# Performance work log

Hardware: AMD Instinct MI355X
Metric: run time of the kernel (lower is better)

The kernel has to match this reference:

```python
import jax, jax.numpy as jnp
import numpy as np

S, B, T, E, H, VS, VT = 40, 32, 40, 256, 512, 50000, 50000
PAD = 0


def lstm_cell(x, h, c, Wih, Whh, b):
    # PyTorch gate order: i, f, g, o
    g = x @ Wih.T + h @ Whh.T + b
    i, f, gg, o = jnp.split(g, 4, axis=-1)
    c = jax.nn.sigmoid(f) * c + jax.nn.sigmoid(i) * jnp.tanh(gg)
    h = jax.nn.sigmoid(o) * jnp.tanh(c)
    return h, c


def run_lstm(xs, Wih, Whh, b):
    # xs: [S, B, E] -> hs [S, B, H], final (h, c)
    b_ = xs.shape[1]
    init = (jnp.zeros((b_, H), xs.dtype), jnp.zeros((b_, H), xs.dtype))
    def step(carry, x):
        h, c = lstm_cell(x, carry[0], carry[1], Wih, Whh, b)
        return (h, c), h
    (hT, cT), hs = jax.lax.scan(step, init, xs)
    return hs, hT, cT


def setup_inputs() -> dict:
    key = jax.random.key(0)
    ks = jax.random.split(key, 20)
    w = lambda k, shp: (jax.random.normal(k, shp, dtype=jnp.float32) * 0.05)
    return {
        "padded_source": jax.random.randint(ks[0], (S, B), 0, VS, dtype=jnp.int32),
        "padded_target": jax.random.randint(ks[1], (T, B), 0, VT, dtype=jnp.int32),
        "enc_masks": jnp.zeros((B, S), dtype=jnp.float32),
        "src_embed": w(ks[2], (VS, E)),
        "tgt_embed": w(ks[3], (VT, E)),
        "enc_Wih_f": w(ks[4], (4 * H, E)),
        "enc_Whh_f": w(ks[5], (4 * H, H)),
        "enc_b_f": w(ks[6], (4 * H,)),
        "enc_Wih_b": w(ks[7], (4 * H, E)),
        "enc_Whh_b": w(ks[8], (4 * H, H)),
        "enc_b_b": w(ks[9], (4 * H,)),
        "dec_Wih": w(ks[10], (4 * H, E + H)),
        "dec_Whh": w(ks[11], (4 * H, H)),
        "dec_b": w(ks[12], (4 * H,)),
        "W_h": w(ks[13], (H, 2 * H)),
        "W_c": w(ks[14], (H, 2 * H)),
        "W_att": w(ks[15], (H, 2 * H)),
        "W_comb": w(ks[16], (H, 3 * H)),
        "W_vocab": w(ks[17], (VT, H)),
    }


def reference(padded_source, padded_target, enc_masks, src_embed, tgt_embed,
              enc_Wih_f, enc_Whh_f, enc_b_f, enc_Wih_b, enc_Whh_b, enc_b_b,
              dec_Wih, dec_Whh, dec_b, W_h, W_c, W_att, W_comb, W_vocab):
    # ---- encode ----
    src_e = src_embed[padded_source]                      # [S, B, E]
    hs_f, hT_f, cT_f = run_lstm(src_e, enc_Wih_f, enc_Whh_f, enc_b_f)
    hs_b, hT_b, cT_b = run_lstm(src_e[::-1], enc_Wih_b, enc_Whh_b, enc_b_b)
    hs_b = hs_b[::-1]
    enc_hidden = jnp.concatenate([hs_f, hs_b], axis=-1).transpose(1, 0, 2)  # [B, S, 2H]
    dec_h = jnp.concatenate([hT_f, hT_b], axis=-1) @ W_h.T  # [B, H]
    dec_c = jnp.concatenate([cT_f, cT_b], axis=-1) @ W_c.T
    enc_proj = enc_hidden @ W_att.T                        # [B, S, H]

    # ---- decode (scan over target timesteps) ----
    tgt_e = tgt_embed[padded_target[:-1]]                  # [T-1, B, E]
    o0 = jnp.zeros((enc_hidden.shape[0], H), enc_hidden.dtype)

    def dstep(carry, emb_t):
        h, c, o_prev = carry
        x = jnp.concatenate([emb_t, o_prev], axis=-1)
        h, c = lstm_cell(x, h, c, dec_Wih, dec_Whh, dec_b)
        scores = jnp.einsum('bsh,bh->bs', enc_proj, h)
        scores = jnp.where(enc_masks > 0, -jnp.inf, scores)
        att = jax.nn.softmax(scores, axis=-1)
        ctx = jnp.einsum('bs,bsd->bd', att, enc_hidden)
        o_t = jnp.tanh(jnp.concatenate([h, ctx], axis=-1) @ W_comb.T)
        return (h, c, o_t), o_t

    _, outs = jax.lax.scan(dstep, (dec_h, dec_c, o0), tgt_e)  # [T-1, B, H]

    # ---- scoring ----
    logp = jax.nn.log_softmax(outs @ W_vocab.T, axis=-1)      # [T-1, B, VT]
    tgt = padded_target[1:]
    tmask = (tgt != PAD).astype(logp.dtype)
    picked = jnp.take_along_axis(logp, tgt[..., None], axis=-1)[..., 0] * tmask
    return picked.sum(axis=0)                                  # [B]
```

## Files before the change

kernel.cpp:

```cpp
#include <hip/hip_runtime.h>
#include <hip/hip_cooperative_groups.h>
#include <math.h>

namespace cg = cooperative_groups;


#define S_LEN 40
#define BATCH 32
#define EMB   256
#define HID   512
#define G4H   2048
#define NVOC  50000
#define NDEC  39
#define NCHUNK 196
#define MROWS 1248
#define MPAD  1280

__device__ __forceinline__ float sigf(float x) { return 1.f / (1.f + expf(-x)); }

__global__ __launch_bounds__(256) void k_embed(
    const int* __restrict__ src_ids, const int* __restrict__ tgt_ids,
    const float* __restrict__ src_emb, const float* __restrict__ tgt_emb,
    float* __restrict__ src_e, float* __restrict__ tgt_e)
{
  int row = blockIdx.x, tid = threadIdx.x;
  if (row < S_LEN*BATCH) {
    int id = src_ids[row];
    src_e[(size_t)row*EMB + tid] = src_emb[(size_t)id*EMB + tid];
  } else {
    int r = row - S_LEN*BATCH;
    int id = tgt_ids[r];
    tgt_e[(size_t)r*EMB + tid] = tgt_emb[(size_t)id*EMB + tid];
  }
}

__global__ __launch_bounds__(256) void k_gemm(
    const float* __restrict__ A, const float* __restrict__ W,
    const float* __restrict__ bias, float* __restrict__ C,
    int N, int K, int ldw, int rev)
{
  __shared__ float As[16][36];
  __shared__ float Ws[16][256];
  const int tid = threadIdx.x;
  const int tx = tid & 31, ty = tid >> 5;
  const int bn = (int)blockIdx.x << 8;
  const int bmi = (int)blockIdx.y;
  const int bm = bmi << 5;
  const int arow0 = rev ? ((S_LEN - 1 - bmi) << 5) : bm;

  float acc[4][8];
#pragma unroll
  for (int i = 0; i < 4; i++)
#pragma unroll
    for (int j = 0; j < 8; j++) acc[i][j] = 0.f;

  const int ml = tid >> 3, kl = (tid & 7) << 1;
  const float* aptr = A + (size_t)(arow0 + ml)*K + kl;
  const float* wptr = W + (size_t)(bn + tid)*ldw;

  for (int k0 = 0; k0 < K; k0 += 16) {
    const float2 av  = *(const float2*)(aptr + k0);
    const float4 w0v = *(const float4*)(wptr + k0);
    const float4 w1v = *(const float4*)(wptr + k0 + 4);
    const float4 w2v = *(const float4*)(wptr + k0 + 8);
    const float4 w3v = *(const float4*)(wptr + k0 + 12);
    __syncthreads();
    As[kl][ml]   = av.x;
    As[kl+1][ml] = av.y;
    const float wt[16] = {w0v.x,w0v.y,w0v.z,w0v.w, w1v.x,w1v.y,w1v.z,w1v.w,
                          w2v.x,w2v.y,w2v.z,w2v.w, w3v.x,w3v.y,w3v.z,w3v.w};
#pragma unroll
    for (int kk = 0; kk < 16; kk++) Ws[kk][tid] = wt[kk];
    __syncthreads();
#pragma unroll
    for (int kk = 0; kk < 16; kk++) {
      const float4 a4 = *(const float4*)&As[kk][ty << 2];
      const float4 b0 = *(const float4*)&Ws[kk][tx << 2];
      const float4 b1 = *(const float4*)&Ws[kk][128 + (tx << 2)];
      const float ar[4] = {a4.x, a4.y, a4.z, a4.w};
      const float br[8] = {b0.x, b0.y, b0.z, b0.w, b1.x, b1.y, b1.z, b1.w};
#pragma unroll
      for (int i = 0; i < 4; i++)
#pragma unroll
        for (int j = 0; j < 8; j++) acc[i][j] += ar[i]*br[j];
    }
  }
  float4 bb0 = {0,0,0,0}, bb1 = {0,0,0,0};
  if (bias) {
    bb0 = *(const float4*)&bias[bn + (tx << 2)];
    bb1 = *(const float4*)&bias[bn + 128 + (tx << 2)];
  }
#pragma unroll
  for (int i = 0; i < 4; i++) {
    const int row = bm + (ty << 2) + i;
    float4 o0 = {acc[i][0]+bb0.x, acc[i][1]+bb0.y, acc[i][2]+bb0.z, acc[i][3]+bb0.w};
    float4 o1 = {acc[i][4]+bb1.x, acc[i][5]+bb1.y, acc[i][6]+bb1.z, acc[i][7]+bb1.w};
    *(float4*)&C[(size_t)row*N + bn + (tx << 2)] = o0;
    *(float4*)&C[(size_t)row*N + bn + 128 + (tx << 2)] = o1;
  }
}

__global__ __launch_bounds__(256) void k_enc(
    const float* __restrict__ xpf, const float* __restrict__ xpb,
    const float* __restrict__ Whf, const float* __restrict__ Whb,
    float* __restrict__ hpf, float* __restrict__ hpb,
    float* __restrict__ hcat, float* __restrict__ ccat)
{
  cg::grid_group grid = cg::this_grid();
  const int blk = blockIdx.x;
  const int dir = blk >> 7;
  const int ub  = blk & 127;
  const int tid = threadIdx.x;
  const int w = tid >> 6, lane = tid & 63;
  const int r = lane & 31, half = lane >> 5;
  const int j = ub*4 + w;
  const int kbase = half << 8;

  const float* xp  = dir ? xpb : xpf;
  const float* Whh = dir ? Whb : Whf;
  float* hp = dir ? hpb : hpf;

  const float* w0 = Whh + (size_t)(0*HID + j)*HID + kbase;
  const float* w1 = Whh + (size_t)(1*HID + j)*HID + kbase;
  const float* w2 = Whh + (size_t)(2*HID + j)*HID + kbase;
  const float* w3 = Whh + (size_t)(3*HID + j)*HID + kbase;

  float creg = 0.f;
  for (int t = 0; t < S_LEN; t++) {
    float a0 = 0.f, a1 = 0.f, a2 = 0.f, a3 = 0.f;
    if (t > 0) {
      const float* hb = hp + (size_t)(t-1)*16384 + (kbase << 5) + (r << 2);
#pragma unroll 4
      for (int kk = 0; kk < 256; kk += 4) {
        const float4 hv = *(const float4*)(hb + (kk << 5));
        const float4 v0 = *(const float4*)(w0 + kk);
        const float4 v1 = *(const float4*)(w1 + kk);
        const float4 v2 = *(const float4*)(w2 + kk);
        const float4 v3 = *(const float4*)(w3 + kk);
        a0 += v0.x*hv.x + v0.y*hv.y + v0.z*hv.z + v0.w*hv.w;
        a1 += v1.x*hv.x + v1.y*hv.y + v1.z*hv.z + v1.w*hv.w;
        a2 += v2.x*hv.x + v2.y*hv.y + v2.z*hv.z + v2.w*hv.w;
        a3 += v3.x*hv.x + v3.y*hv.y + v3.z*hv.z + v3.w*hv.w;
      }
    }
    a0 += __shfl_down(a0, 32);
    a1 += __shfl_down(a1, 32);
    a2 += __shfl_down(a2, 32);
    a3 += __shfl_down(a3, 32);
    if (half == 0) {
      const float* xrow = xp + (size_t)(t*BATCH + r)*G4H;
      const float gi = a0 + xrow[j];
      const float gf = a1 + xrow[HID + j];
      const float gg = a2 + xrow[2*HID + j];
      const float go = a3 + xrow[3*HID + j];
      const float cn = sigf(gf)*creg + sigf(gi)*tanhf(gg);
      const float hn = sigf(go)*tanhf(cn);
      creg = cn;
      hp[(size_t)t*16384 + (j >> 2)*128 + (r << 2) + (j & 3)] = hn;
      if (t == S_LEN-1) {
        hcat[r*1024 + dir*HID + j] = hn;
        ccat[r*1024 + dir*HID + j] = cn;
      }
    }
    grid.sync();
  }
}

__global__ __launch_bounds__(256) void k_concat(
    const float* __restrict__ hpf, const float* __restrict__ hpb,
    float* __restrict__ ench)
{
  const int blk = blockIdx.x, tid = threadIdx.x;
  const int b = blk / S_LEN, s = blk - b*S_LEN;
#pragma unroll
  for (int q = 0; q < 4; q++) {
    const int d = tid + (q << 8);
    float v;
    if (d < HID) v = hpf[(size_t)s*16384 + (d >> 2)*128 + (b << 2) + (d & 3)];
    else {
      const int d2 = d - HID;
      v = hpb[(size_t)(S_LEN-1-s)*16384 + (d2 >> 2)*128 + (b << 2) + (d2 & 3)];
    }
    ench[(size_t)blk*1024 + d] = v;
  }
}

__global__ __launch_bounds__(256) void k_dec(
    const float* __restrict__ xproj, const float* __restrict__ Wih, const float* __restrict__ Whh,
    const float* __restrict__ Wcomb, const float* __restrict__ encp, const float* __restrict__ ench,
    const float* __restrict__ masks, const float* __restrict__ h0, const float* __restrict__ c0,
    float* __restrict__ aop, float* __restrict__ xcomb, float* __restrict__ outs)
{
  cg::grid_group grid = cg::this_grid();
  __shared__ float redA[4][2][4][32];
  __shared__ float redC[4][2][32];
  __shared__ float hl[HID];
  __shared__ float sc[S_LEN];

  const int blk = blockIdx.x, tid = threadIdx.x;
  const int w = tid >> 6, lane = tid & 63;
  const int r = lane & 31, half = lane >> 5;
  const int j0 = blk*2;

  const int kbA = w*256 + half*128;
  const float* wA[8];
#pragma unroll
  for (int u = 0; u < 2; u++)
#pragma unroll
    for (int g = 0; g < 4; g++) {
      const int row = g*HID + j0 + u;
      wA[u*4+g] = (kbA < HID) ? (Wih + (size_t)row*768 + 256 + kbA)
                              : (Whh + (size_t)row*HID + (kbA - HID));
    }
  const float* habase = aop + (kbA << 5) + (r << 2);

  const int kbC = w*384 + half*192;
  const float* wC0 = Wcomb + (size_t)(j0  )*1536 + kbC;
  const float* wC1 = Wcomb + (size_t)(j0+1)*1536 + kbC;
  const float* hcbase = xcomb + (kbC << 5) + (r << 2);

  float creg = 0.f;
  if (tid < 64) {
    const int uh = tid >> 5, rr = tid & 31;
    const int j = j0 + uh;
    creg = c0[rr*HID + j];
    aop[(128 + (j >> 2))*128 + (rr << 2) + (j & 3)] = h0[rr*HID + j];
    aop[((j >> 2))*128 + (rr << 2) + (j & 3)] = 0.f;
  }
  grid.sync();

  for (int t = 0; t < NDEC; t++) {
    {
      float acc8[8];
#pragma unroll
      for (int p = 0; p < 8; p++) acc8[p] = 0.f;
#pragma unroll 2
      for (int kk = 0; kk < 128; kk += 4) {
        const float4 hv = *(const float4*)(habase + (kk << 5));
#pragma unroll
        for (int p = 0; p < 8; p++) {
          const float4 wv = *(const float4*)(wA[p] + kk);
          acc8[p] += wv.x*hv.x + wv.y*hv.y + wv.z*hv.z + wv.w*hv.w;
        }
      }
#pragma unroll
      for (int p = 0; p < 8; p++) acc8[p] += __shfl_down(acc8[p], 32);
      if (half == 0) {
#pragma unroll
        for (int p = 0; p < 8; p++) redA[w][p >> 2][p & 3][r] = acc8[p];
      }
    }
    __syncthreads();
    if (tid < 64) {
      const int uh = tid >> 5, rr = tid & 31, j = j0 + uh;
      const float* xrow = xproj + (size_t)(t*BATCH + rr)*G4H;
      float g4[4];
#pragma unroll
      for (int g = 0; g < 4; g++)
        g4[g] = xrow[g*HID + j] + redA[0][uh][g][rr] + redA[1][uh][g][rr]
                                + redA[2][uh][g][rr] + redA[3][uh][g][rr];
      const float cn = sigf(g4[1])*creg + sigf(g4[0])*tanhf(g4[2]);
      const float hn = sigf(g4[3])*tanhf(cn);
      creg = cn;
      xcomb[(j >> 2)*128 + (rr << 2) + (j & 3)] = hn;
      aop[(128 + (j >> 2))*128 + (rr << 2) + (j & 3)] = hn;
    }
    grid.sync();

    if (blk < BATCH) {
      const int b = blk;
      if (tid < 128) ((float4*)hl)[tid] = *(const float4*)&xcomb[tid*128 + (b << 2)];
      __syncthreads();
      for (int s = w; s < S_LEN; s += 4) {
        const float* ep = encp + ((size_t)b*S_LEN + s)*HID;
        float part = 0.f;
#pragma unroll
        for (int k = 0; k < 8; k++) part += ep[lane + (k << 6)]*hl[lane + (k << 6)];
#pragma unroll
        for (int m = 32; m >= 1; m >>= 1) part += __shfl_xor(part, m, 64);
        if (lane == 0) sc[s] = (masks[b*S_LEN + s] > 0.f) ? -INFINITY : part;
      }
      __syncthreads();
      float mx = -INFINITY;
      for (int s2 = 0; s2 < S_LEN; s2++) mx = fmaxf(mx, sc[s2]);
      float sm = 0.f;
      for (int s2 = 0; s2 < S_LEN; s2++) sm += expf(sc[s2] - mx);
      const float inv = 1.f/sm;
      const float myatt = (tid < S_LEN) ? expf(sc[tid] - mx)*inv : 0.f;
      __syncthreads();
      if (tid < S_LEN) sc[tid] = myatt;
      __syncthreads();
#pragma unroll
      for (int q = 0; q < 4; q++) {
        const int d = tid + (q << 8);
        float cd = 0.f;
        for (int s = 0; s < S_LEN; s++) cd += sc[s]*ench[((size_t)b*S_LEN + s)*1024 + d];
        const int k = HID + d;
        xcomb[(k >> 2)*128 + (b << 2) + (k & 3)] = cd;
      }
    }
    grid.sync();

    {
      float ca = 0.f, cb = 0.f;
#pragma unroll 2
      for (int kk = 0; kk < 192; kk += 4) {
        const float4 hv = *(const float4*)(hcbase + (kk << 5));
        const float4 v0 = *(const float4*)(wC0 + kk);
        const float4 v1 = *(const float4*)(wC1 + kk);
        ca += v0.x*hv.x + v0.y*hv.y + v0.z*hv.z + v0.w*hv.w;
        cb += v1.x*hv.x + v1.y*hv.y + v1.z*hv.z + v1.w*hv.w;
      }
      ca += __shfl_down(ca, 32);
      cb += __shfl_down(cb, 32);
      if (half == 0) { redC[w][0][r] = ca; redC[w][1][r] = cb; }
    }
    __syncthreads();
    if (tid < 64) {
      const int uh = tid >> 5, rr = tid & 31, j = j0 + uh;
      const float o = tanhf(redC[0][uh][rr] + redC[1][uh][rr] + redC[2][uh][rr] + redC[3][uh][rr]);
      aop[(j >> 2)*128 + (rr << 2) + (j & 3)] = o;
      outs[(size_t)(t*BATCH + rr)*HID + j] = o;
    }
    grid.sync();
  }
}

__global__ __launch_bounds__(256) void k_vocab(
    const float* __restrict__ A, const float* __restrict__ W,
    const int* __restrict__ ptgt,
    float* __restrict__ pmax, float* __restrict__ psum, float* __restrict__ picked)
{
  __shared__ float As[16][68];
  __shared__ float Ws[16][256];
  const int tid = threadIdx.x;
  const int tx = tid & 31, ty = tid >> 5;
  const int bn = (int)blockIdx.x << 8;
  const int bm = (int)blockIdx.y << 6;

  float acc[8][8];
#pragma unroll
  for (int i = 0; i < 8; i++)
#pragma unroll
    for (int j = 0; j < 8; j++) acc[i][j] = 0.f;

  const int ml = tid >> 2, kl = (tid & 3) << 2;
  const float* aptr = A + (size_t)(bm + ml)*HID + kl;
  int wrow = bn + tid; if (wrow >= NVOC) wrow = NVOC - 1;
  const float* wptr = W + (size_t)wrow*HID;

  for (int k0 = 0; k0 < HID; k0 += 16) {
    const float4 av  = *(const float4*)(aptr + k0);
    const float4 w0v = *(const float4*)(wptr + k0);
    const float4 w1v = *(const float4*)(wptr + k0 + 4);
    const float4 w2v = *(const float4*)(wptr + k0 + 8);
    const float4 w3v = *(const float4*)(wptr + k0 + 12);
    __syncthreads();
    As[kl][ml] = av.x; As[kl+1][ml] = av.y; As[kl+2][ml] = av.z; As[kl+3][ml] = av.w;
    const float wt[16] = {w0v.x,w0v.y,w0v.z,w0v.w, w1v.x,w1v.y,w1v.z,w1v.w,
                          w2v.x,w2v.y,w2v.z,w2v.w, w3v.x,w3v.y,w3v.z,w3v.w};
#pragma unroll
    for (int kk = 0; kk < 16; kk++) Ws[kk][tid] = wt[kk];
    __syncthreads();
#pragma unroll
    for (int kk = 0; kk < 16; kk++) {
      const float4 a0 = *(const float4*)&As[kk][ty << 3];
      const float4 a1 = *(const float4*)&As[kk][(ty << 3) + 4];
      const float4 b0 = *(const float4*)&Ws[kk][tx << 2];
      const float4 b1 = *(const float4*)&Ws[kk][128 + (tx << 2)];
      const float ar[8] = {a0.x,a0.y,a0.z,a0.w, a1.x,a1.y,a1.z,a1.w};
      const float br[8] = {b0.x,b0.y,b0.z,b0.w, b1.x,b1.y,b1.z,b1.w};
#pragma unroll
      for (int i = 0; i < 8; i++)
#pragma unroll
        for (int j = 0; j < 8; j++) acc[i][j] += ar[i]*br[j];
    }
  }
#pragma unroll
  for (int i = 0; i < 8; i++) {
    const int row = bm + (ty << 3) + i;
    float mx = -INFINITY;
#pragma unroll
    for (int j = 0; j < 8; j++) {
      const int col = bn + ((j < 4) ? (tx << 2) + j : 128 + (tx << 2) + j - 4);
      if (col < NVOC) mx = fmaxf(mx, acc[i][j]);
    }
#pragma unroll
    for (int m = 16; m >= 1; m >>= 1) mx = fmaxf(mx, __shfl_xor(mx, m, 32));
    float sm = 0.f;
#pragma unroll
    for (int j = 0; j < 8; j++) {
      const int col = bn + ((j < 4) ? (tx << 2) + j : 128 + (tx << 2) + j - 4);
      if (col < NVOC) sm += expf(acc[i][j] - mx);
    }
#pragma unroll
    for (int m = 16; m >= 1; m >>= 1) sm += __shfl_xor(sm, m, 32);
    if (tx == 0) {
      pmax[(size_t)row*NCHUNK + blockIdx.x] = mx;
      psum[(size_t)row*NCHUNK + blockIdx.x] = sm;
    }
    if (row < MROWS) {
      const int tt = row >> 5, bb = row & 31;
      const int tv = ptgt[(tt + 1)*BATCH + bb];
      const int rel = tv - bn;
      if (rel >= 0 && rel < 256) {
#pragma unroll
        for (int j = 0; j < 8; j++) {
          const int cl = (j < 4) ? (tx << 2) + j : 128 + (tx << 2) + j - 4;
          if (cl == rel) picked[row] = acc[i][j];
        }
      }
    }
  }
}

__global__ __launch_bounds__(256) void k_final(
    const float* __restrict__ pmax, const float* __restrict__ psum,
    const float* __restrict__ picked, const int* __restrict__ ptgt,
    float* __restrict__ out)
{
  __shared__ float red[8];
  const int b = (int)blockIdx.x, tid = threadIdx.x;
  const int lane = tid & 63, w = tid >> 6;
  float accum = 0.f;
  for (int t = 0; t < NDEC; t++) {
    const int row = t*BATCH + b;
    const float* pm = pmax + (size_t)row*NCHUNK;
    const float* ps = psum + (size_t)row*NCHUNK;
    float mx = -INFINITY;
    for (int c = tid; c < NCHUNK; c += 256) mx = fmaxf(mx, pm[c]);
#pragma unroll
    for (int m = 32; m >= 1; m >>= 1) mx = fmaxf(mx, __shfl_xor(mx, m, 64));
    if (lane == 0) red[w] = mx;
    __syncthreads();
    mx = fmaxf(fmaxf(red[0], red[1]), fmaxf(red[2], red[3]));
    __syncthreads();
    float sm = 0.f;
    for (int c = tid; c < NCHUNK; c += 256) sm += ps[c]*expf(pm[c] - mx);
#pragma unroll
    for (int m = 32; m >= 1; m >>= 1) sm += __shfl_xor(sm, m, 64);
    if (lane == 0) red[w] = sm;
    __syncthreads();
    sm = red[0] + red[1] + red[2] + red[3];
    __syncthreads();
    if (tid == 0) {
      const int tv = ptgt[(t + 1)*BATCH + b];
      if (tv != 0) accum += picked[row] - (mx + logf(sm));
    }
  }
  if (tid == 0) out[b] = accum;
}

extern "C" void kernel_launch(void* const* d_in, const int* in_sizes, int n_in,
                              void* d_out, int out_size, void* d_ws, size_t ws_size,
                              hipStream_t stream) {
  (void)in_sizes; (void)n_in; (void)out_size; (void)ws_size;
  const int*   p_src     = (const int*)d_in[0];
  const int*   p_tgt     = (const int*)d_in[1];
  const float* enc_masks = (const float*)d_in[2];
  const float* src_embed = (const float*)d_in[3];
  const float* tgt_embed = (const float*)d_in[4];
  const float* Wih_f = (const float*)d_in[5];
  const float* Whh_f = (const float*)d_in[6];
  const float* b_f   = (const float*)d_in[7];
  const float* Wih_b = (const float*)d_in[8];
  const float* Whh_b = (const float*)d_in[9];
  const float* b_b   = (const float*)d_in[10];
  const float* dWih  = (const float*)d_in[11];
  const float* dWhh  = (const float*)d_in[12];
  const float* db    = (const float*)d_in[13];
  const float* W_h   = (const float*)d_in[14];
  const float* W_c   = (const float*)d_in[15];
  const float* W_att = (const float*)d_in[16];
  const float* W_comb= (const float*)d_in[17];
  const float* W_voc = (const float*)d_in[18];
  float* out = (float*)d_out;

  float* p = (float*)d_ws;
  float* src_e    = p; p += S_LEN*BATCH*EMB;
  float* tgt_e    = p; p += NDEC*BATCH*EMB;
  float* xpf      = p; p += S_LEN*BATCH*G4H;
  float* xpb      = p; p += S_LEN*BATCH*G4H;
  float* dec_xp   = p; p += NDEC*BATCH*G4H;
  float* hpf      = p; p += S_LEN*BATCH*HID;
  float* hpb      = p; p += S_LEN*BATCH*HID;
  float* hcat     = p; p += BATCH*2*HID;
  float* ccat     = p; p += BATCH*2*HID;
  float* ench     = p; p += BATCH*S_LEN*2*HID;
  float* encp     = p; p += BATCH*S_LEN*HID;
  float* h0       = p; p += BATCH*HID;
  float* c0       = p; p += BATCH*HID;
  float* aop      = p; p += 1024*BATCH;
  float* xcomb    = p; p += 1536*BATCH;
  float* outs     = p; p += (size_t)MPAD*HID;
  float* pmaxb    = p; p += (size_t)MPAD*NCHUNK;
  float* psumb    = p; p += (size_t)MPAD*NCHUNK;
  float* pickedb  = p; p += MPAD;

  k_embed<<<S_LEN*BATCH + NDEC*BATCH, 256, 0, stream>>>(p_src, p_tgt, src_embed, tgt_embed, src_e, tgt_e);

  k_gemm<<<dim3(8, 40), 256, 0, stream>>>(src_e, Wih_f, b_f, xpf, G4H, EMB, EMB, 0);
  k_gemm<<<dim3(8, 40), 256, 0, stream>>>(src_e, Wih_b, b_b, xpb, G4H, EMB, EMB, 1);
  k_gemm<<<dim3(8, NDEC), 256, 0, stream>>>(tgt_e, dWih, db, dec_xp, G4H, EMB, 768, 0);

  {
    void* args[] = { (void*)&xpf, (void*)&xpb, (void*)&Whh_f, (void*)&Whh_b,
                     (void*)&hpf, (void*)&hpb, (void*)&hcat, (void*)&ccat };
    hipLaunchCooperativeKernel((void*)k_enc, dim3(256), dim3(256), args, 0, stream);
  }

  k_concat<<<BATCH*S_LEN, 256, 0, stream>>>(hpf, hpb, ench);

  k_gemm<<<dim3(2, 40), 256, 0, stream>>>(ench, W_att, nullptr, encp, HID, 2*HID, 2*HID, 0);
  k_gemm<<<dim3(2, 1), 256, 0, stream>>>(hcat, W_h, nullptr, h0, HID, 2*HID, 2*HID, 0);
  k_gemm<<<dim3(2, 1), 256, 0, stream>>>(ccat, W_c, nullptr, c0, HID, 2*HID, 2*HID, 0);

  {
    void* args[] = { (void*)&dec_xp, (void*)&dWih, (void*)&dWhh, (void*)&W_comb,
                     (void*)&encp, (void*)&ench, (void*)&enc_masks, (void*)&h0, (void*)&c0,
                     (void*)&aop, (void*)&xcomb, (void*)&outs };
    hipLaunchCooperativeKernel((void*)k_dec, dim3(256), dim3(256), args, 0, stream);
  }

  k_vocab<<<dim3(NCHUNK, MPAD/64), 256, 0, stream>>>(outs, W_voc, p_tgt, pmaxb, psumb, pickedb);
  k_final<<<32, 256, 0, stream>>>(pmaxb, psumb, pickedb, p_tgt, out);
}
```

Baseline: 9.120 ms.

## Replace cooperative grid-sync recurrences with per-batch blocks and bf16 MFMA vocab GEMM

```diff
diff --git a/kernel.cpp b/kernel.cpp
--- a/kernel.cpp
+++ b/kernel.cpp
@@ -1,8 +1,5 @@
 #include <hip/hip_runtime.h>
-#include <hip/hip_cooperative_groups.h>
 #include <math.h>
-
-namespace cg = cooperative_groups;
 
 
 #define S_LEN 40
@@ -16,7 +13,14 @@
 #define MROWS 1248
 #define MPAD  1280
 
+typedef __attribute__((ext_vector_type(8))) short short8v;
+typedef __attribute__((ext_vector_type(4))) float f32x4;
+
 __device__ __forceinline__ float sigf(float x) { return 1.f / (1.f + expf(-x)); }
+__device__ __forceinline__ unsigned short f2bf(float x) {
+  unsigned u = __float_as_uint(x);
+  return (unsigned short)((u + 0x7fffu + ((u >> 16) & 1u)) >> 16);
+}
 
 __global__ __launch_bounds__(256) void k_embed(
     const int* __restrict__ src_ids, const int* __restrict__ tgt_ids,
@@ -103,85 +107,61 @@
 __global__ __launch_bounds__(256) void k_enc(
     const float* __restrict__ xpf, const float* __restrict__ xpb,
     const float* __restrict__ Whf, const float* __restrict__ Whb,
-    float* __restrict__ hpf, float* __restrict__ hpb,
-    float* __restrict__ hcat, float* __restrict__ ccat)
-{
-  cg::grid_group grid = cg::this_grid();
+    float* __restrict__ ench, float* __restrict__ hcat, float* __restrict__ ccat)
+{
+  __shared__ float hl[HID];
   const int blk = blockIdx.x;
-  const int dir = blk >> 7;
-  const int ub  = blk & 127;
+  const int dir = blk >> 5, b = blk & 31;
   const int tid = threadIdx.x;
-  const int w = tid >> 6, lane = tid & 63;
-  const int r = lane & 31, half = lane >> 5;
-  const int j = ub*4 + w;
-  const int kbase = half << 8;
-
   const float* xp  = dir ? xpb : xpf;
   const float* Whh = dir ? Whb : Whf;
-  float* hp = dir ? hpb : hpf;
-
-  const float* w0 = Whh + (size_t)(0*HID + j)*HID + kbase;
-  const float* w1 = Whh + (size_t)(1*HID + j)*HID + kbase;
-  const float* w2 = Whh + (size_t)(2*HID + j)*HID + kbase;
-  const float* w3 = Whh + (size_t)(3*HID + j)*HID + kbase;
-
-  float creg = 0.f;
+
+  const float* wp[8];
+#pragma unroll
+  for (int u = 0; u < 2; u++)
+#pragma unroll
+    for (int g = 0; g < 4; g++)
+      wp[u*4+g] = Whh + (size_t)(g*HID + tid + u*256)*HID;
+
+  float creg[2] = {0.f, 0.f};
   for (int t = 0; t < S_LEN; t++) {
-    float a0 = 0.f, a1 = 0.f, a2 = 0.f, a3 = 0.f;
+    float a8[8] = {0,0,0,0,0,0,0,0};
     if (t > 0) {
-      const float* hb = hp + (size_t)(t-1)*16384 + (kbase << 5) + (r << 2);
-#pragma unroll 4
-      for (int kk = 0; kk < 256; kk += 4) {
-        const float4 hv = *(const float4*)(hb + (kk << 5));
-        const float4 v0 = *(const float4*)(w0 + kk);
-        const float4 v1 = *(const float4*)(w1 + kk);
-        const float4 v2 = *(const float4*)(w2 + kk);
-        const float4 v3 = *(const float4*)(w3 + kk);
-        a0 += v0.x*hv.x + v0.y*hv.y + v0.z*hv.z + v0.w*hv.w;
-        a1 += v1.x*hv.x + v1.y*hv.y + v1.z*hv.z + v1.w*hv.w;
-        a2 += v2.x*hv.x + v2.y*hv.y + v2.z*hv.z + v2.w*hv.w;
-        a3 += v3.x*hv.x + v3.y*hv.y + v3.z*hv.z + v3.w*hv.w;
-      }
-    }
-    a0 += __shfl_down(a0, 32);
-    a1 += __shfl_down(a1, 32);
-    a2 += __shfl_down(a2, 32);
-    a3 += __shfl_down(a3, 32);
-    if (half == 0) {
-      const float* xrow = xp + (size_t)(t*BATCH + r)*G4H;
-      const float gi = a0 + xrow[j];
-      const float gf = a1 + xrow[HID + j];
-      const float gg = a2 + xrow[2*HID + j];
-      const float go = a3 + xrow[3*HID + j];
-      const float cn = sigf(gf)*creg + sigf(gi)*tanhf(gg);
+      for (int k = 0; k < HID; k += 4) {
+        const float4 hv = *(const float4*)&hl[k];
+#pragma unroll
+        for (int p = 0; p < 8; p++) {
+          const float4 w4 = *(const float4*)(wp[p] + k);
+          a8[p] += w4.x*hv.x + w4.y*hv.y + w4.z*hv.z + w4.w*hv.w;
+        }
+      }
+    }
+    const float* xrow = xp + (size_t)(t*BATCH + b)*G4H;
+    const int s = dir ? (S_LEN-1-t) : t;
+    float hn2[2];
+#pragma unroll
+    for (int u = 0; u < 2; u++) {
+      const int j = tid + u*256;
+      const float gi = a8[u*4+0] + xrow[j];
+      const float gf = a8[u*4+1] + xrow[HID + j];
+      const float gg = a8[u*4+2] + xrow[2*HID + j];
+      const float go = a8[u*4+3] + xrow[3*HID + j];
+      const float cn = sigf(gf)*creg[u] + sigf(gi)*tanhf(gg);
       const float hn = sigf(go)*tanhf(cn);
-      creg = cn;
-      hp[(size_t)t*16384 + (j >> 2)*128 + (r << 2) + (j & 3)] = hn;
-      if (t == S_LEN-1) {
-        hcat[r*1024 + dir*HID + j] = hn;
-        ccat[r*1024 + dir*HID + j] = cn;
-      }
-    }
-    grid.sync();
-  }
-}
-
-__global__ __launch_bounds__(256) void k_concat(
-    const float* __restrict__ hpf, const float* __restrict__ hpb,
-    float* __restrict__ ench)
-{
-  const int blk = blockIdx.x, tid = threadIdx.x;
-  const int b = blk / S_LEN, s = blk - b*S_LEN;
-#pragma unroll
-  for (int q = 0; q < 4; q++) {
-    const int d = tid + (q << 8);
-    float v;
-    if (d < HID) v = hpf[(size_t)s*16384 + (d >> 2)*128 + (b << 2) + (d & 3)];
-    else {
-      const int d2 = d - HID;
-      v = hpb[(size_t)(S_LEN-1-s)*16384 + (d2 >> 2)*128 + (b << 2) + (d2 & 3)];
-    }
-    ench[(size_t)blk*1024 + d] = v;
+      creg[u] = cn; hn2[u] = hn;
+      ench[((size_t)b*S_LEN + s)*1024 + dir*HID + j] = hn;
+    }
+    __syncthreads();
+    hl[tid] = hn2[0]; hl[tid+256] = hn2[1];
+    __syncthreads();
+    if (t == S_LEN-1) {
+#pragma unroll
+      for (int u = 0; u < 2; u++) {
+        const int j = tid + u*256;
+        hcat[b*1024 + dir*HID + j] = hn2[u];
+        ccat[b*1024 + dir*HID + j] = creg[u];
+      }
+    }
   }
 }
 
@@ -189,227 +169,217 @@
     const float* __restrict__ xproj, const float* __restrict__ Wih, const float* __restrict__ Whh,
     const float* __restrict__ Wcomb, const float* __restrict__ encp, const float* __restrict__ ench,
     const float* __restrict__ masks, const float* __restrict__ h0, const float* __restrict__ c0,
-    float* __restrict__ aop, float* __restrict__ xcomb, float* __restrict__ outs)
-{
-  cg::grid_group grid = cg::this_grid();
-  __shared__ float redA[4][2][4][32];
-  __shared__ float redC[4][2][32];
-  __shared__ float hl[HID];
-  __shared__ float sc[S_LEN];
-
-  const int blk = blockIdx.x, tid = threadIdx.x;
-  const int w = tid >> 6, lane = tid & 63;
-  const int r = lane & 31, half = lane >> 5;
-  const int j0 = blk*2;
-
-  const int kbA = w*256 + half*128;
-  const float* wA[8];
+    unsigned short* __restrict__ obf)
+{
+  __shared__ float xa[1024];
+  __shared__ float ctx[1024];
+  __shared__ float scr[S_LEN], sc2[S_LEN];
+  const int b = blockIdx.x, tid = threadIdx.x;
+  const int l = tid & 63, wv = tid >> 6;
+
+  const float* wihp[8]; const float* whhp[8];
 #pragma unroll
   for (int u = 0; u < 2; u++)
 #pragma unroll
     for (int g = 0; g < 4; g++) {
-      const int row = g*HID + j0 + u;
-      wA[u*4+g] = (kbA < HID) ? (Wih + (size_t)row*768 + 256 + kbA)
-                              : (Whh + (size_t)row*HID + (kbA - HID));
-    }
-  const float* habase = aop + (kbA << 5) + (r << 2);
-
-  const int kbC = w*384 + half*192;
-  const float* wC0 = Wcomb + (size_t)(j0  )*1536 + kbC;
-  const float* wC1 = Wcomb + (size_t)(j0+1)*1536 + kbC;
-  const float* hcbase = xcomb + (kbC << 5) + (r << 2);
-
-  float creg = 0.f;
-  if (tid < 64) {
-    const int uh = tid >> 5, rr = tid & 31;
-    const int j = j0 + uh;
-    creg = c0[rr*HID + j];
-    aop[(128 + (j >> 2))*128 + (rr << 2) + (j & 3)] = h0[rr*HID + j];
-    aop[((j >> 2))*128 + (rr << 2) + (j & 3)] = 0.f;
-  }
-  grid.sync();
+      const int row = g*HID + tid + u*256;
+      wihp[u*4+g] = Wih + (size_t)row*768 + 256;
+      whhp[u*4+g] = Whh + (size_t)row*HID;
+    }
+  const float* wcp[2] = { Wcomb + (size_t)tid*1536, Wcomb + (size_t)(tid+256)*1536 };
+
+  float creg[2] = { c0[b*HID + tid], c0[b*HID + tid + 256] };
+  xa[tid] = 0.f; xa[tid+256] = 0.f;
+  xa[512 + tid] = h0[b*HID + tid];
+  xa[512 + tid + 256] = h0[b*HID + tid + 256];
+  __syncthreads();
 
   for (int t = 0; t < NDEC; t++) {
+    float a8[8] = {0,0,0,0,0,0,0,0};
+    for (int k = 0; k < HID; k += 4) {
+      const float4 xv = *(const float4*)&xa[k];
+#pragma unroll
+      for (int p = 0; p < 8; p++) {
+        const float4 w4 = *(const float4*)(wihp[p] + k);
+        a8[p] += w4.x*xv.x + w4.y*xv.y + w4.z*xv.z + w4.w*xv.w;
+      }
+    }
+    for (int k = 0; k < HID; k += 4) {
+      const float4 xv = *(const float4*)&xa[512 + k];
+#pragma unroll
+      for (int p = 0; p < 8; p++) {
+        const float4 w4 = *(const float4*)(whhp[p] + k);
+        a8[p] += w4.x*xv.x + w4.y*xv.y + w4.z*xv.z + w4.w*xv.w;
+      }
+    }
+    const float* xrow = xproj + (size_t)(t*BATCH + b)*G4H;
+    float hn2[2];
+#pragma unroll
+    for (int u = 0; u < 2; u++) {
+      const int j = tid + u*256;
+      const float gi = a8[u*4+0] + xrow[j];
+      const float gf = a8[u*4+1] + xrow[HID + j];
+      const float gg = a8[u*4+2] + xrow[2*HID + j];
+      const float go = a8[u*4+3] + xrow[3*HID + j];
+      const float cn = sigf(gf)*creg[u] + sigf(gi)*tanhf(gg);
+      const float hn = sigf(go)*tanhf(cn);
+      creg[u] = cn; hn2[u] = hn;
+    }
+    __syncthreads();
+    xa[512 + tid] = hn2[0]; xa[512 + tid + 256] = hn2[1];
+    __syncthreads();
+
+    for (int s = wv; s < S_LEN; s += 4) {
+      const float* ep = encp + ((size_t)b*S_LEN + s)*HID;
+      float part = 0.f;
+#pragma unroll
+      for (int kk = 0; kk < 8; kk++) part += ep[l + (kk << 6)] * xa[512 + l + (kk << 6)];
+#pragma unroll
+      for (int m = 32; m >= 1; m >>= 1) part += __shfl_xor(part, m, 64);
+      if (l == 0) scr[s] = (masks[b*S_LEN + s] > 0.f) ? -INFINITY : part;
+    }
+    __syncthreads();
     {
-      float acc8[8];
-#pragma unroll
-      for (int p = 0; p < 8; p++) acc8[p] = 0.f;
-#pragma unroll 2
-      for (int kk = 0; kk < 128; kk += 4) {
-        const float4 hv = *(const float4*)(habase + (kk << 5));
-#pragma unroll
-        for (int p = 0; p < 8; p++) {
-          const float4 wv = *(const float4*)(wA[p] + kk);
-          acc8[p] += wv.x*hv.x + wv.y*hv.y + wv.z*hv.z + wv.w*hv.w;
-        }
-      }
-#pragma unroll
-      for (int p = 0; p < 8; p++) acc8[p] += __shfl_down(acc8[p], 32);
-      if (half == 0) {
-#pragma unroll
-        for (int p = 0; p < 8; p++) redA[w][p >> 2][p & 3][r] = acc8[p];
-      }
-    }
-    __syncthreads();
-    if (tid < 64) {
-      const int uh = tid >> 5, rr = tid & 31, j = j0 + uh;
-      const float* xrow = xproj + (size_t)(t*BATCH + rr)*G4H;
-      float g4[4];
-#pragma unroll
-      for (int g = 0; g < 4; g++)
-        g4[g] = xrow[g*HID + j] + redA[0][uh][g][rr] + redA[1][uh][g][rr]
-                                + redA[2][uh][g][rr] + redA[3][uh][g][rr];
-      const float cn = sigf(g4[1])*creg + sigf(g4[0])*tanhf(g4[2]);
-      const float hn = sigf(g4[3])*tanhf(cn);
-      creg = cn;
-      xcomb[(j >> 2)*128 + (rr << 2) + (j & 3)] = hn;
-      aop[(128 + (j >> 2))*128 + (rr << 2) + (j & 3)] = hn;
-    }
-    grid.sync();
-
-    if (blk < BATCH) {
-      const int b = blk;
-      if (tid < 128) ((float4*)hl)[tid] = *(const float4*)&xcomb[tid*128 + (b << 2)];
-      __syncthreads();
-      for (int s = w; s < S_LEN; s += 4) {
-        const float* ep = encp + ((size_t)b*S_LEN + s)*HID;
-        float part = 0.f;
-#pragma unroll
-        for (int k = 0; k < 8; k++) part += ep[lane + (k << 6)]*hl[lane + (k << 6)];
-#pragma unroll
-        for (int m = 32; m >= 1; m >>= 1) part += __shfl_xor(part, m, 64);
-        if (lane == 0) sc[s] = (masks[b*S_LEN + s] > 0.f) ? -INFINITY : part;
-      }
-      __syncthreads();
       float mx = -INFINITY;
-      for (int s2 = 0; s2 < S_LEN; s2++) mx = fmaxf(mx, sc[s2]);
+      for (int s = 0; s < S_LEN; s++) mx = fmaxf(mx, scr[s]);
       float sm = 0.f;
-      for (int s2 = 0; s2 < S_LEN; s2++) sm += expf(sc[s2] - mx);
+      for (int s = 0; s < S_LEN; s++) sm += expf(scr[s] - mx);
       const float inv = 1.f/sm;
-      const float myatt = (tid < S_LEN) ? expf(sc[tid] - mx)*inv : 0.f;
-      __syncthreads();
-      if (tid < S_LEN) sc[tid] = myatt;
-      __syncthreads();
-#pragma unroll
-      for (int q = 0; q < 4; q++) {
-        const int d = tid + (q << 8);
-        float cd = 0.f;
-        for (int s = 0; s < S_LEN; s++) cd += sc[s]*ench[((size_t)b*S_LEN + s)*1024 + d];
-        const int k = HID + d;
-        xcomb[(k >> 2)*128 + (b << 2) + (k & 3)] = cd;
-      }
-    }
-    grid.sync();
-
-    {
-      float ca = 0.f, cb = 0.f;
-#pragma unroll 2
-      for (int kk = 0; kk < 192; kk += 4) {
-        const float4 hv = *(const float4*)(hcbase + (kk << 5));
-        const float4 v0 = *(const float4*)(wC0 + kk);
-        const float4 v1 = *(const float4*)(wC1 + kk);
-        ca += v0.x*hv.x + v0.y*hv.y + v0.z*hv.z + v0.w*hv.w;
-        cb += v1.x*hv.x + v1.y*hv.y + v1.z*hv.z + v1.w*hv.w;
-      }
-      ca += __shfl_down(ca, 32);
-      cb += __shfl_down(cb, 32);
-      if (half == 0) { redC[w][0][r] = ca; redC[w][1][r] = cb; }
-    }
-    __syncthreads();
-    if (tid < 64) {
-      const int uh = tid >> 5, rr = tid & 31, j = j0 + uh;
-      const float o = tanhf(redC[0][uh][rr] + redC[1][uh][rr] + redC[2][uh][rr] + redC[3][uh][rr]);
-      aop[(j >> 2)*128 + (rr << 2) + (j & 3)] = o;
-      outs[(size_t)(t*BATCH + rr)*HID + j] = o;
-    }
-    grid.sync();
-  }
+      if (tid < S_LEN) sc2[tid] = expf(scr[tid] - mx)*inv;
+    }
+    __syncthreads();
+#pragma unroll
+    for (int q = 0; q < 4; q++) {
+      const int d = tid + (q << 8);
+      float cd = 0.f;
+      for (int s = 0; s < S_LEN; s++) cd += sc2[s]*ench[((size_t)b*S_LEN + s)*1024 + d];
+      ctx[d] = cd;
+    }
+    __syncthreads();
+
+#pragma unroll
+    for (int u = 0; u < 2; u++) {
+      const float* wr = wcp[u];
+      float a = 0.f;
+      for (int k = 0; k < HID; k += 4) {
+        const float4 w4 = *(const float4*)(wr + k);
+        const float4 h4 = *(const float4*)&xa[512 + k];
+        a += w4.x*h4.x + w4.y*h4.y + w4.z*h4.z + w4.w*h4.w;
+      }
+      for (int k = 0; k < 1024; k += 4) {
+        const float4 w4 = *(const float4*)(wr + HID + k);
+        const float4 c4 = *(const float4*)&ctx[k];
+        a += w4.x*c4.x + w4.y*c4.y + w4.z*c4.z + w4.w*c4.w;
+      }
+      const float o = tanhf(a);
+      const int j = tid + u*256;
+      xa[j] = o;
+      obf[(size_t)(t*BATCH + b)*HID + j] = f2bf(o);
+    }
+    __syncthreads();
+  }
+}
+
+__global__ __launch_bounds__(256) void k_zero_bf(unsigned short* __restrict__ p) {
+  p[(size_t)MROWS*HID + blockIdx.x*256 + threadIdx.x] = 0;
 }
 
 __global__ __launch_bounds__(256) void k_vocab(
-    const float* __restrict__ A, const float* __restrict__ W,
+    const unsigned short* __restrict__ Ab, const float* __restrict__ Wv,
     const int* __restrict__ ptgt,
     float* __restrict__ pmax, float* __restrict__ psum, float* __restrict__ picked)
 {
-  __shared__ float As[16][68];
-  __shared__ float Ws[16][256];
+  __shared__ char ldsbuf[133120];
+  __shared__ float redm[2][128], reds[2][128];
+  short* Af = (short*)ldsbuf;
+  float* Cs = (float*)ldsbuf;
+
   const int tid = threadIdx.x;
-  const int tx = tid & 31, ty = tid >> 5;
-  const int bn = (int)blockIdx.x << 8;
-  const int bm = (int)blockIdx.y << 6;
-
-  float acc[8][8];
-#pragma unroll
-  for (int i = 0; i < 8; i++)
-#pragma unroll
-    for (int j = 0; j < 8; j++) acc[i][j] = 0.f;
-
-  const int ml = tid >> 2, kl = (tid & 3) << 2;
-  const float* aptr = A + (size_t)(bm + ml)*HID + kl;
-  int wrow = bn + tid; if (wrow >= NVOC) wrow = NVOC - 1;
-  const float* wptr = W + (size_t)wrow*HID;
-
-  for (int k0 = 0; k0 < HID; k0 += 16) {
-    const float4 av  = *(const float4*)(aptr + k0);
-    const float4 w0v = *(const float4*)(wptr + k0);
-    const float4 w1v = *(const float4*)(wptr + k0 + 4);
-    const float4 w2v = *(const float4*)(wptr + k0 + 8);
-    const float4 w3v = *(const float4*)(wptr + k0 + 12);
-    __syncthreads();
-    As[kl][ml] = av.x; As[kl+1][ml] = av.y; As[kl+2][ml] = av.z; As[kl+3][ml] = av.w;
-    const float wt[16] = {w0v.x,w0v.y,w0v.z,w0v.w, w1v.x,w1v.y,w1v.z,w1v.w,
-                          w2v.x,w2v.y,w2v.z,w2v.w, w3v.x,w3v.y,w3v.z,w3v.w};
-#pragma unroll
-    for (int kk = 0; kk < 16; kk++) Ws[kk][tid] = wt[kk];
-    __syncthreads();
-#pragma unroll
-    for (int kk = 0; kk < 16; kk++) {
-      const float4 a0 = *(const float4*)&As[kk][ty << 3];
-      const float4 a1 = *(const float4*)&As[kk][(ty << 3) + 4];
-      const float4 b0 = *(const float4*)&Ws[kk][tx << 2];
-      const float4 b1 = *(const float4*)&Ws[kk][128 + (tx << 2)];
-      const float ar[8] = {a0.x,a0.y,a0.z,a0.w, a1.x,a1.y,a1.z,a1.w};
-      const float br[8] = {b0.x,b0.y,b0.z,b0.w, b1.x,b1.y,b1.z,b1.w};
-#pragma unroll
-      for (int i = 0; i < 8; i++)
-#pragma unroll
-        for (int j = 0; j < 8; j++) acc[i][j] += ar[i]*br[j];
-    }
-  }
-#pragma unroll
-  for (int i = 0; i < 8; i++) {
-    const int row = bm + (ty << 3) + i;
-    float mx = -INFINITY;
-#pragma unroll
-    for (int j = 0; j < 8; j++) {
-      const int col = bn + ((j < 4) ? (tx << 2) + j : 128 + (tx << 2) + j - 4);
-      if (col < NVOC) mx = fmaxf(mx, acc[i][j]);
-    }
-#pragma unroll
-    for (int m = 16; m >= 1; m >>= 1) mx = fmaxf(mx, __shfl_xor(mx, m, 32));
-    float sm = 0.f;
-#pragma unroll
-    for (int j = 0; j < 8; j++) {
-      const int col = bn + ((j < 4) ? (tx << 2) + j : 128 + (tx << 2) + j - 4);
-      if (col < NVOC) sm += expf(acc[i][j] - mx);
-    }
-#pragma unroll
-    for (int m = 16; m >= 1; m >>= 1) sm += __shfl_xor(sm, m, 32);
-    if (tx == 0) {
-      pmax[(size_t)row*NCHUNK + blockIdx.x] = mx;
-      psum[(size_t)row*NCHUNK + blockIdx.x] = sm;
-    }
-    if (row < MROWS) {
-      const int tt = row >> 5, bb = row & 31;
-      const int tv = ptgt[(tt + 1)*BATCH + bb];
+  const int l = tid & 63, wq = tid >> 6;
+  const int bx = (int)blockIdx.x, bm = (int)blockIdx.y << 7;
+  const int bn = bx << 8;
+
+#pragma unroll
+  for (int i = 0; i < 32; i++) {
+    const int s = tid + (i << 8);
+    const int f = s >> 6, ln = s & 63;
+    const int row = ((f >> 4) << 4) + (ln & 15);
+    const int koff = ((f & 15) << 5) + ((ln >> 4) << 3);
+    *(short8v*)&Af[s*8] = *(const short8v*)&Ab[(size_t)(bm + row)*HID + koff];
+  }
+  __syncthreads();
+
+  const float* bptr[4];
+#pragma unroll
+  for (int nt = 0; nt < 4; nt++) {
+    int rowv = bn + wq*64 + nt*16 + (l & 15);
+    if (rowv > NVOC-1) rowv = NVOC-1;
+    bptr[nt] = Wv + (size_t)rowv*HID + ((l >> 4) << 3);
+  }
+
+  f32x4 acc[8][4];
+#pragma unroll
+  for (int mt = 0; mt < 8; mt++)
+#pragma unroll
+    for (int nt = 0; nt < 4; nt++) acc[mt][nt] = (f32x4){0.f,0.f,0.f,0.f};
+
+  for (int ks = 0; ks < 16; ks++) {
+    short8v bfr[4];
+#pragma unroll
+    for (int nt = 0; nt < 4; nt++) {
+      const float4 wa = *(const float4*)(bptr[nt] + ks*32);
+      const float4 wb = *(const float4*)(bptr[nt] + ks*32 + 4);
+      union { int i[4]; short8v s; } u;
+      u.i[0] = __builtin_amdgcn_perm(__float_as_uint(wa.y), __float_as_uint(wa.x), 0x07060302);
+      u.i[1] = __builtin_amdgcn_perm(__float_as_uint(wa.w), __float_as_uint(wa.z), 0x07060302);
+      u.i[2] = __builtin_amdgcn_perm(__float_as_uint(wb.y), __float_as_uint(wb.x), 0x07060302);
+      u.i[3] = __builtin_amdgcn_perm(__float_as_uint(wb.w), __float_as_uint(wb.z), 0x07060302);
+      bfr[nt] = u.s;
+    }
+#pragma unroll
+    for (int mt = 0; mt < 8; mt++) {
+      const short8v af = *(const short8v*)&Af[((mt*16 + ks)*64 + l)*8];
+#pragma unroll
+      for (int nt = 0; nt < 4; nt++)
+        acc[mt][nt] = __builtin_amdgcn_mfma_f32_16x16x32_bf16(af, bfr[nt], acc[mt][nt], 0, 0, 0);
+    }
+  }
+
+  __syncthreads();
+#pragma unroll
+  for (int mt = 0; mt < 8; mt++)
+#pragma unroll
+    for (int nt = 0; nt < 4; nt++) {
+      const int row = mt*16 + (l >> 4)*4;
+      const int col = wq*64 + nt*16 + (l & 15);
+#pragma unroll
+      for (int r = 0; r < 4; r++)
+        Cs[(row + r)*260 + col] = acc[mt][nt][r];
+    }
+  __syncthreads();
+
+  const int row = tid & 127, half = tid >> 7;
+  const float* crow = Cs + row*260 + half*128;
+  const int colbase = bn + half*128;
+  float mx = -INFINITY;
+  for (int i = 0; i < 128; i++)
+    if (colbase + i < NVOC) mx = fmaxf(mx, crow[i]);
+  redm[half][row] = mx;
+  __syncthreads();
+  const float rmx = fmaxf(redm[0][row], redm[1][row]);
+  float sm = 0.f;
+  for (int i = 0; i < 128; i++)
+    if (colbase + i < NVOC) sm += expf(crow[i] - rmx);
+  reds[half][row] = sm;
+  __syncthreads();
+  if (half == 0) {
+    const int rowg = bm + row;
+    pmax[(size_t)rowg*NCHUNK + bx] = rmx;
+    psum[(size_t)rowg*NCHUNK + bx] = reds[0][row] + reds[1][row];
+    if (rowg < MROWS) {
+      const int tv = ptgt[((rowg >> 5) + 1)*BATCH + (rowg & 31)];
       const int rel = tv - bn;
-      if (rel >= 0 && rel < 256) {
-#pragma unroll
-        for (int j = 0; j < 8; j++) {
-          const int cl = (j < 4) ? (tx << 2) + j : 128 + (tx << 2) + j - 4;
-          if (cl == rel) picked[row] = acc[i][j];
-        }
-      }
+      if (rel >= 0 && rel < 256) picked[rowg] = Cs[row*260 + rel];
     }
   }
 }
@@ -482,17 +452,13 @@
   float* xpf      = p; p += S_LEN*BATCH*G4H;
   float* xpb      = p; p += S_LEN*BATCH*G4H;
   float* dec_xp   = p; p += NDEC*BATCH*G4H;
-  float* hpf      = p; p += S_LEN*BATCH*HID;
-  float* hpb      = p; p += S_LEN*BATCH*HID;
+  float* ench     = p; p += BATCH*S_LEN*2*HID;
+  float* encp     = p; p += BATCH*S_LEN*HID;
   float* hcat     = p; p += BATCH*2*HID;
   float* ccat     = p; p += BATCH*2*HID;
-  float* ench     = p; p += BATCH*S_LEN*2*HID;
-  float* encp     = p; p += BATCH*S_LEN*HID;
   float* h0       = p; p += BATCH*HID;
   float* c0       = p; p += BATCH*HID;
-  float* aop      = p; p += 1024*BATCH;
-  float* xcomb    = p; p += 1536*BATCH;
-  float* outs     = p; p += (size_t)MPAD*HID;
+  unsigned short* outs_bf = (unsigned short*)p; p += (size_t)MPAD*HID/2;
   float* pmaxb    = p; p += (size_t)MPAD*NCHUNK;
   float* psumb    = p; p += (size_t)MPAD*NCHUNK;
   float* pickedb  = p; p += MPAD;
@@ -503,25 +469,15 @@
   k_gemm<<<dim3(8, 40), 256, 0, stream>>>(src_e, Wih_b, b_b, xpb, G4H, EMB, EMB, 1);
   k_gemm<<<dim3(8, NDEC), 256, 0, stream>>>(tgt_e, dWih, db, dec_xp, G4H, EMB, 768, 0);
 
-  {
-    void* args[] = { (void*)&xpf, (void*)&xpb, (void*)&Whh_f, (void*)&Whh_b,
-                     (void*)&hpf, (void*)&hpb, (void*)&hcat, (void*)&ccat };
-    hipLaunchCooperativeKernel((void*)k_enc, dim3(256), dim3(256), args, 0, stream);
-  }
-
-  k_concat<<<BATCH*S_LEN, 256, 0, stream>>>(hpf, hpb, ench);
+  k_enc<<<64, 256, 0, stream>>>(xpf, xpb, Whh_f, Whh_b, ench, hcat, ccat);
 
   k_gemm<<<dim3(2, 40), 256, 0, stream>>>(ench, W_att, nullptr, encp, HID, 2*HID, 2*HID, 0);
   k_gemm<<<dim3(2, 1), 256, 0, stream>>>(hcat, W_h, nullptr, h0, HID, 2*HID, 2*HID, 0);
   k_gemm<<<dim3(2, 1), 256, 0, stream>>>(ccat, W_c, nullptr, c0, HID, 2*HID, 2*HID, 0);
 
-  {
-    void* args[] = { (void*)&dec_xp, (void*)&dWih, (void*)&dWhh, (void*)&W_comb,
-                     (void*)&encp, (void*)&ench, (void*)&enc_masks, (void*)&h0, (void*)&c0,
-                     (void*)&aop, (void*)&xcomb, (void*)&outs };
-    hipLaunchCooperativeKernel((void*)k_dec, dim3(256), dim3(256), args, 0, stream);
-  }
-
-  k_vocab<<<dim3(NCHUNK, MPAD/64), 256, 0, stream>>>(outs, W_voc, p_tgt, pmaxb, psumb, pickedb);
+  k_dec<<<32, 256, 0, stream>>>(dec_xp, dWih, dWhh, W_comb, encp, ench, enc_masks, h0, c0, outs_bf);
+
+  k_zero_bf<<<(MPAD-MROWS)*HID/256, 256, 0, stream>>>(outs_bf);
+  k_vocab<<<dim3(NCHUNK, MPAD/128), 256, 0, stream>>>(outs_bf, W_voc, p_tgt, pmaxb, psumb, pickedb);
   k_final<<<32, 256, 0, stream>>>(pmaxb, psumb, pickedb, p_tgt, out);
 }
```

Result: slower. 19.71 ms (+116.1%).
